# Kernel optimization log

Hardware: AMD Instinct MI355X
Metric: run time of the kernel (lower is better)

## Reference

```python
import jax, jax.numpy as jnp
import numpy as np

N = 100000   # nodes
E = 1600000  # edges (before self loops)
F = 64       # num_features
H = 64       # hidden_channels
C = 10       # num_classes
G = 128      # graphs in batch
NEG_SLOPE = 0.2


def setup_inputs() -> dict:
    key = jax.random.key(0)
    ks = jax.random.split(key, 16)
    x = jax.random.normal(ks[0], (N, F), dtype=jnp.float32)
    edge_index = jax.random.randint(ks[1], (2, E), 0, N, dtype=jnp.int64)
    batch = jnp.sort(jax.random.randint(ks[2], (N,), 0, G, dtype=jnp.int64))
    def glorot(k, shape):
        fan = shape[0] + shape[-1]
        return jax.random.uniform(k, shape, jnp.float32, -1.0, 1.0) * np.sqrt(6.0 / fan)
    return {
        "x": x, "edge_index": edge_index, "batch": batch,
        # GATConv 1 (F -> H)
        "W1": glorot(ks[3], (F, H)), "as1": glorot(ks[4], (H,)), "ad1": glorot(ks[5], (H,)), "b1": jnp.zeros((H,), jnp.float32),
        # GATConv 2 (H -> H)
        "W2": glorot(ks[6], (H, H)), "as2": glorot(ks[7], (H,)), "ad2": glorot(ks[8], (H,)), "b2": jnp.zeros((H,), jnp.float32),
        # MLP head
        "mw1": glorot(ks[9], (H, H)), "mb1": jnp.zeros((H,), jnp.float32),
        "mw2": glorot(ks[10], (H, C)), "mb2": jnp.zeros((C,), jnp.float32),
    }


def gat_conv(x, src, dst, W, a_s, a_d, b):
    # x: [N, Fin] -> h: [N, Fout]
    h = x @ W
    # per-node attention halves, gathered per edge (heads=1)
    al_s = h @ a_s   # [N]
    al_d = h @ a_d   # [N]
    e = jax.nn.leaky_relu(al_s[src] + al_d[dst], NEG_SLOPE)  # [E']
    # segment softmax over incoming edges of each destination node
    m = jax.ops.segment_max(e, dst, num_segments=N)
    ex = jnp.exp(e - m[dst])
    denom = jax.ops.segment_sum(ex, dst, num_segments=N)
    alpha = ex / denom[dst]                                   # [E']
    # weighted scatter-add of source features
    out = jax.ops.segment_sum(alpha[:, None] * h[src], dst, num_segments=N)
    return out + b


def reference(x, edge_index, batch, W1, as1, ad1, b1, W2, as2, ad2, b2, mw1, mb1, mw2, mb2):
    # add self loops (PyG GATConv default)
    loop = jnp.arange(N, dtype=edge_index.dtype)
    src = jnp.concatenate([edge_index[0], loop])
    dst = jnp.concatenate([edge_index[1], loop])

    h = gat_conv(x, src, dst, W1, as1, ad1, b1)
    h = jax.nn.elu(h)  # dropout p=0.5 is identity in eval mode
    h = gat_conv(h, src, dst, W2, as2, ad2, b2)
    h = jax.nn.elu(h)

    h = jax.nn.relu(h @ mw1 + mb1) @ mw2 + mb2   # MLP [N, C]
    return jax.ops.segment_sum(h, batch, num_segments=G)  # global_add_pool [G, C]
```

## Files before the change

### kernel.cpp

```cpp
#include <hip/hip_runtime.h>
#include <hip/hip_bf16.h>
#include <math.h>

#define SHIFT 20.0f
#define T_PER 8
#define TILE (256 * T_PER)
#define SEG_CAP 12288
#define BCAP 10240
#define LS_T 1024

typedef __bf16 bf16x8 __attribute__((ext_vector_type(8)));
typedef float  f32x4  __attribute__((ext_vector_type(4)));

__device__ __forceinline__ unsigned f2bf(float f) {
    unsigned u = __float_as_uint(f);
    return (u + 0x7fffu + ((u >> 16) & 1u)) >> 16;
}

__global__ void setup_kernel(int* __restrict__ bcur, int K2,
                             float* __restrict__ Pz, int nPz,
                             const float* __restrict__ W1,
                             const float* __restrict__ as1, const float* __restrict__ ad1,
                             const float* __restrict__ W2,
                             const float* __restrict__ as2, const float* __restrict__ ad2,
                             const float* __restrict__ mw1,
                             uint4* __restrict__ Wf1, uint4* __restrict__ Wf2,
                             uint4* __restrict__ mwf)
{
    int t = threadIdx.x;
    if (blockIdx.x == 0) {
        if (t < K2) bcur[t * 16] = t * BCAP;
        for (int i = t; i < nPz; i += 256) Pz[i] = 0.f;
        return;
    }
    __shared__ float wasad[256];
    {
        int k = t & 63;
        const float* W  = (t < 128) ? W1 : W2;
        const float* av = (t < 64) ? as1 : (t < 128) ? ad1 : (t < 192) ? as2 : ad2;
        float s = 0.f;
        for (int n = 0; n < 64; n++) s = fmaf(W[k * 64 + n], av[n], s);
        wasad[t] = s;
    }
    __syncthreads();

    for (int idx = t; idx < 1792; idx += 256) {
        const float* W; const float* wv; uint4* dst; int rem;
        if (idx < 640)       { rem = idx;        W = W1;  wv = &wasad[0];   dst = Wf1; }
        else if (idx < 1280) { rem = idx - 640;  W = W2;  wv = &wasad[128]; dst = Wf2; }
        else                 { rem = idx - 1280; W = mw1; wv = nullptr;     dst = mwf; }
        int pair = rem >> 6, l = rem & 63;
        int tt = pair >> 1, s = pair & 1;
        int kb = s * 32 + (l >> 4) * 8;
        unsigned d[4];
        if (tt < 4) {
            int n = tt * 16 + (l & 15);
            #pragma unroll
            for (int j = 0; j < 4; j++)
                d[j] = f2bf(W[(kb + 2 * j) * 64 + n]) |
                       (f2bf(W[(kb + 2 * j + 1) * 64 + n]) << 16);
        } else {
            int n0 = l & 15;
            #pragma unroll
            for (int j = 0; j < 4; j++) {
                float v0 = (n0 == 0) ? wv[kb + 2 * j]     : (n0 == 1) ? wv[64 + kb + 2 * j]     : 0.f;
                float v1 = (n0 == 0) ? wv[kb + 2 * j + 1] : (n0 == 1) ? wv[64 + kb + 2 * j + 1] : 0.f;
                d[j] = f2bf(v0) | (f2bf(v1) << 16);
            }
        }
        dst[pair * 64 + l] = make_uint4(d[0], d[1], d[2], d[3]);
    }
}

__device__ __forceinline__ void multisplit_body(
    unsigned char* lds, const int* __restrict__ esrc, const int* __restrict__ edst,
    int* __restrict__ bcur, unsigned* __restrict__ pairbuf,
    int nE, int tot, int K2, int tile)
{
    int* lhist = (int*)lds;
    int* lbase = lhist + 256;
    int t = threadIdx.x;
    int base = tile * TILE;
    if (t < K2) lhist[t] = 0;
    __syncthreads();

    unsigned pk[T_PER];
    int loc[T_PER];
    #pragma unroll
    for (int i = 0; i < T_PER; i++) {
        int e = base + t + i * 256;
        if (e < tot) {
            int s = (e < nE) ? esrc[e] : (e - nE);
            int d = (e < nE) ? edst[e] : (e - nE);
            int b = d >> 9;
            pk[i] = ((unsigned)s << 9) | (unsigned)(d & 511);
            int idx = atomicAdd(&lhist[b], 1);
            loc[i] = (b << 20) | idx;
        } else loc[i] = -1;
    }
    __syncthreads();
    if (t < K2) {
        int c = lhist[t];
        lbase[t] = (c > 0) ? atomicAdd(&bcur[t * 16], c) : 0;
    }
    __syncthreads();
    #pragma unroll
    for (int i = 0; i < T_PER; i++) {
        if (loc[i] >= 0)
            pairbuf[lbase[loc[i] >> 20] + (loc[i] & 0xFFFFF)] = pk[i];
    }
}

__device__ __forceinline__ void gemm_body(
    unsigned char* lds, const void* __restrict__ Xv, int x_is_bf16,
    const uint4* __restrict__ Wf, __hip_bfloat16* __restrict__ Hout,
    float* __restrict__ als, float* __restrict__ ald, int nN, int b0)
{
    int t = threadIdx.x, lane = t & 63, wv = t >> 6;

    uint4 wf[10];
    #pragma unroll
    for (int p = 0; p < 10; p++) wf[p] = Wf[p * 64 + lane];

    if (x_is_bf16) {
        const uint4* X4 = (const uint4*)Xv;
        int limit = nN * 8;
        #pragma unroll
        for (int k = 0; k < 8; k++) {
            int dst = t + k * 256;
            int idx = b0 * 8 + dst;
            if (idx < limit) {
                int r = dst >> 3, c = dst & 7;
                *(uint4*)(lds + r * 144 + c * 16) = X4[idx];
            }
        }
    } else {
        const float4* Xf = (const float4*)Xv;
        int limit = nN * 16;
        #pragma unroll
        for (int k = 0; k < 16; k++) {
            int dst = t + k * 256;
            int idx = b0 * 16 + dst;
            if (idx < limit) {
                float4 v = Xf[idx];
                uint2 r2;
                r2.x = f2bf(v.x) | (f2bf(v.y) << 16);
                r2.y = f2bf(v.z) | (f2bf(v.w) << 16);
                int r = dst >> 4, c = dst & 15;
                *(uint2*)(lds + r * 144 + c * 8) = r2;
            }
        }
    }
    __syncthreads();

    f32x4 acc[4][5] = {};
    int rbase = wv * 64;
    #pragma unroll
    for (int s = 0; s < 2; s++) {
        #pragma unroll
        for (int rf = 0; rf < 4; rf++) {
            const uint4 av = *(const uint4*)(lds + (rbase + rf * 16 + (lane & 15)) * 144
                                                 + s * 64 + (lane >> 4) * 16);
            bf16x8 a = __builtin_bit_cast(bf16x8, av);
            #pragma unroll
            for (int tt = 0; tt < 5; tt++) {
                bf16x8 b = __builtin_bit_cast(bf16x8, wf[tt * 2 + s]);
                acc[rf][tt] = __builtin_amdgcn_mfma_f32_16x16x32_bf16(a, b, acc[rf][tt], 0, 0, 0);
            }
        }
    }

    int q = lane >> 4, c = lane & 15;
    #pragma unroll
    for (int rf = 0; rf < 4; rf++) {
        #pragma unroll
        for (int r = 0; r < 4; r++) {
            int n = b0 + rbase + rf * 16 + q * 4 + r;
            if (n < nN) {
                #pragma unroll
                for (int tt = 0; tt < 4; tt++)
                    Hout[(size_t)n * 64 + tt * 16 + c] = __float2bfloat16(acc[rf][tt][r]);
                if (c == 0)      als[n] = acc[rf][4][r];
                else if (c == 1) ald[n] = acc[rf][4][r];
            }
        }
    }
}

__global__ __launch_bounds__(256) void ms_gemm_kernel(
    const int* __restrict__ esrc, const int* __restrict__ edst,
    int* __restrict__ bcur, unsigned* __restrict__ pairbuf,
    int nE, int nN, int K2, int nTiles,
    const void* __restrict__ Xv, const uint4* __restrict__ Wf,
    __hip_bfloat16* __restrict__ Hout,
    float* __restrict__ als, float* __restrict__ ald)
{
    __shared__ __align__(16) unsigned char lds[256 * 144];
    if (blockIdx.x < nTiles) {
        multisplit_body(lds, esrc, edst, bcur, pairbuf, nE, nE + nN, K2, blockIdx.x);
    } else {
        gemm_body(lds, Xv, 0, Wf, Hout, als, ald, nN, (blockIdx.x - nTiles) * 256);
    }
}

__global__ __launch_bounds__(256) void gemm_att_mfma(
    const void* __restrict__ Xv, int x_is_bf16,
    const uint4* __restrict__ Wf,
    __hip_bfloat16* __restrict__ Hout,
    float* __restrict__ als, float* __restrict__ ald, int nN)
{
    __shared__ __align__(16) unsigned char lds[256 * 144];
    gemm_body(lds, Xv, x_is_bf16, Wf, Hout, als, ald, nN, blockIdx.x * 256);
}

__global__ __launch_bounds__(LS_T) void local_scatter_kernel(
    const unsigned* __restrict__ pairbuf, const int* __restrict__ bcur,
    int2* __restrict__ rp2, int* __restrict__ csr_src, int nN, int K2)
{
    __shared__ unsigned seg[SEG_CAP];
    __shared__ int lh[512];
    __shared__ int cur[512];
    __shared__ int psum[512];
    int b = blockIdx.x;
    int t = threadIdx.x;
    int d0 = b * 512;
    int nd = min(512, nN - d0);
    int lo = b * BCAP;
    int hi = bcur[b * 16];
    int len = hi - lo;
    bool inLds = (len <= SEG_CAP);

    if (t < 512) lh[t] = 0;
    if (inLds)
        for (int j = t; j < len; j += LS_T) seg[j] = pairbuf[lo + j];
    __syncthreads();
    if (inLds) {
        for (int j = t; j < len; j += LS_T) atomicAdd(&lh[seg[j] & 511u], 1);
    } else {
        for (int j = lo + t; j < hi; j += LS_T)
            atomicAdd(&lh[pairbuf[j] & 511u], 1);
    }
    __syncthreads();

    int v = (t < 512) ? lh[t] : 0;
    if (t < 512) psum[t] = v;
    __syncthreads();
    for (int off = 1; off < 512; off <<= 1) {
        int u = (t < 512 && t >= off) ? psum[t - off] : 0;
        __syncthreads();
        if (t < 512) psum[t] += u;
        __syncthreads();
    }
    if (t < 512) {
        int e0 = lo + psum[t] - v;
        cur[t] = e0;
        if (t < nd) rp2[d0 + t] = make_int2(e0, v);
    }
    __syncthreads();

    if (inLds) {
        for (int j = t; j < len; j += LS_T) {
            unsigned w = seg[j];
            int pos = atomicAdd(&cur[w & 511u], 1);
            csr_src[pos] = (int)(w >> 9);
        }
    } else {
        for (int j = lo + t; j < hi; j += LS_T) {
            unsigned w = pairbuf[j];
            int pos = atomicAdd(&cur[w & 511u], 1);
            csr_src[pos] = (int)(w >> 9);
        }
    }
}

__global__ __launch_bounds__(256) void pull_kernel(
    const int* __restrict__ csr_src, const int2* __restrict__ rp2,
    const unsigned* __restrict__ Hu,
    const float* __restrict__ als, const float* __restrict__ ald,
    const float* __restrict__ bias,
    __hip_bfloat162* __restrict__ out2, int nN)
{
    int lane = threadIdx.x & 63;
    int half = lane >> 5;
    int fl = lane & 31;
    int wid  = (blockIdx.x * blockDim.x + threadIdx.x) >> 6;
    int nw   = (gridDim.x * blockDim.x) >> 6;
    float2 bl2 = ((const float2*)bias)[fl];

    for (int d = wid; d < nN; d += nw) {
        int2 rp = rp2[d];
        int s0 = rp.x, s1 = rp.x + rp.y;
        float aldd = ald[d];
        float aclo = 0.f, achi = 0.f, den = 0.f;

        for (int base = s0; base < s1; base += 64) {
            int j = base + lane;
            bool v = (j < s1);
            int sl = v ? csr_src[j] : 0;
            float ex = 0.f;
            if (v) {
                float sc = als[sl] + aldd;
                sc = (sc > 0.f) ? sc : 0.2f * sc;
                ex = __expf(sc - SHIFT);
            }
            float es = ex;
            #pragma unroll
            for (int off = 32; off > 0; off >>= 1) es += __shfl_xor(es, off);
            den += es;

            int m = min(64, s1 - base);
            int i2 = 0;
            for (; i2 + 3 < m; i2 += 4) {
                int iA = i2 + half, iB = i2 + 2 + half;
                int sA = __shfl(sl, iA), sB = __shfl(sl, iB);
                float eA = __shfl(ex, iA), eB = __shfl(ex, iB);
                unsigned dA = Hu[(size_t)sA * 32 + fl];
                unsigned dB = Hu[(size_t)sB * 32 + fl];
                aclo = fmaf(eA, __uint_as_float(dA << 16), aclo);
                achi = fmaf(eA, __uint_as_float(dA & 0xffff0000u), achi);
                aclo = fmaf(eB, __uint_as_float(dB << 16), aclo);
                achi = fmaf(eB, __uint_as_float(dB & 0xffff0000u), achi);
            }
            for (; i2 < m; i2 += 2) {
                int idx = i2 + half;
                int s = __shfl(sl, idx);
                float e = (idx < m) ? __shfl(ex, idx) : 0.f;
                unsigned dd = Hu[(size_t)s * 32 + fl];
                aclo = fmaf(e, __uint_as_float(dd << 16), aclo);
                achi = fmaf(e, __uint_as_float(dd & 0xffff0000u), achi);
            }
        }
        aclo += __shfl_xor(aclo, 32);
        achi += __shfl_xor(achi, 32);
        float v0 = aclo / den + bl2.x;
        float v1 = achi / den + bl2.y;
        v0 = (v0 > 0.f) ? v0 : expm1f(v0);
        v1 = (v1 > 0.f) ? v1 : expm1f(v1);
        if (half == 0) {
            __hip_bfloat162 pk;
            pk.x = __float2bfloat16(v0);
            pk.y = __float2bfloat16(v1);
            out2[(size_t)d * 32 + fl] = pk;
        }
    }
}

__global__ __launch_bounds__(256) void mlp_pool_mfma(
    const uint4* __restrict__ Hin,
    const uint4* __restrict__ mwf, const float* __restrict__ mb1,
    const int* __restrict__ batch,
    float* __restrict__ P, float* __restrict__ Pcnt, int nN)
{
    __shared__ __align__(16) unsigned char lds[256 * 144];
    int t = threadIdx.x, lane = t & 63, wv = t >> 6;
    int b0 = blockIdx.x * 256;

    uint4 wf[8];
    #pragma unroll
    for (int p = 0; p < 8; p++) wf[p] = mwf[p * 64 + lane];

    int limit = nN * 8;
    #pragma unroll
    for (int k = 0; k < 8; k++) {
        int dst = t + k * 256;
        int idx = b0 * 8 + dst;
        if (idx < limit) {
            int r = dst >> 3, c = dst & 7;
            *(uint4*)(lds + r * 144 + c * 16) = Hin[idx];
        }
    }
    __syncthreads();

    f32x4 acc[4][4] = {};
    int rbase = wv * 64;
    #pragma unroll
    for (int s = 0; s < 2; s++) {
        #pragma unroll
        for (int rf = 0; rf < 4; rf++) {
            const uint4 av = *(const uint4*)(lds + (rbase + rf * 16 + (lane & 15)) * 144
                                                 + s * 64 + (lane >> 4) * 16);
            bf16x8 a = __builtin_bit_cast(bf16x8, av);
            #pragma unroll
            for (int tt = 0; tt < 4; tt++) {
                bf16x8 b = __builtin_bit_cast(bf16x8, wf[tt * 2 + s]);
                acc[rf][tt] = __builtin_amdgcn_mfma_f32_16x16x32_bf16(a, b, acc[rf][tt], 0, 0, 0);
            }
        }
    }

    int q = lane >> 4, c = lane & 15;
    float bl0 = mb1[c], bl1 = mb1[16 + c], bl2 = mb1[32 + c], bl3 = mb1[48 + c];
    float r0 = 0.f, r1 = 0.f, r2 = 0.f, r3 = 0.f, ccnt = 0.f;
    int gcur = -1;
    #pragma unroll
    for (int rf = 0; rf < 4; rf++) {
        #pragma unroll
        for (int r = 0; r < 4; r++) {
            int n = b0 + rbase + rf * 16 + q * 4 + r;
            if (n < nN) {
                int g = batch[n];
                if (g != gcur) {
                    if (gcur >= 0) {
                        atomicAdd(&P[(size_t)gcur * 64 + c],      r0);
                        atomicAdd(&P[(size_t)gcur * 64 + 16 + c], r1);
                        atomicAdd(&P[(size_t)gcur * 64 + 32 + c], r2);
                        atomicAdd(&P[(size_t)gcur * 64 + 48 + c], r3);
                        if (c == 0) atomicAdd(&Pcnt[gcur], ccnt);
                    }
                    gcur = g; r0 = r1 = r2 = r3 = 0.f; ccnt = 0.f;
                }
                r0 += fmaxf(acc[rf][0][r] + bl0, 0.f);
                r1 += fmaxf(acc[rf][1][r] + bl1, 0.f);
                r2 += fmaxf(acc[rf][2][r] + bl2, 0.f);
                r3 += fmaxf(acc[rf][3][r] + bl3, 0.f);
                ccnt += 1.f;
            }
        }
    }
    if (gcur >= 0) {
        atomicAdd(&P[(size_t)gcur * 64 + c],      r0);
        atomicAdd(&P[(size_t)gcur * 64 + 16 + c], r1);
        atomicAdd(&P[(size_t)gcur * 64 + 32 + c], r2);
        atomicAdd(&P[(size_t)gcur * 64 + 48 + c], r3);
        if (c == 0) atomicAdd(&Pcnt[gcur], ccnt);
    }
}

__global__ void head_out_kernel(const float* __restrict__ P,
                                const float* __restrict__ Pcnt,
                                const float* __restrict__ mw2,
                                const float* __restrict__ mb2,
                                float* __restrict__ out, int nOut)
{
    int t = blockIdx.x * blockDim.x + threadIdx.x;
    if (t >= nOut) return;
    int g = t / 10, j = t % 10;
    float s = mb2[j] * Pcnt[g];
    const float* pr = P + (size_t)g * 64;
    #pragma unroll
    for (int k = 0; k < 64; k++) s = fmaf(pr[k], mw2[k * 10 + j], s);
    out[t] = s;
}

extern "C" void kernel_launch(void* const* d_in, const int* in_sizes, int n_in,
                              void* d_out, int out_size, void* d_ws, size_t ws_size,
                              hipStream_t stream)
{
    const float* x   = (const float*)d_in[0];
    const int*  eidx = (const int*)d_in[1];
    const int* batch = (const int*)d_in[2];
    const float* W1  = (const float*)d_in[3];
    const float* as1 = (const float*)d_in[4];
    const float* ad1 = (const float*)d_in[5];
    const float* b1  = (const float*)d_in[6];
    const float* W2  = (const float*)d_in[7];
    const float* as2 = (const float*)d_in[8];
    const float* ad2 = (const float*)d_in[9];
    const float* b2  = (const float*)d_in[10];
    const float* mw1 = (const float*)d_in[11];
    const float* mb1 = (const float*)d_in[12];
    const float* mw2 = (const float*)d_in[13];
    const float* mb2 = (const float*)d_in[14];
    float* out = (float*)d_out;

    int nN = in_sizes[0] / 64;
    int nE = in_sizes[1] / 2;
    int tot = nE + nN;
    int K2 = (nN + 511) >> 9;
    int G  = out_size / 10;
    const int* esrc = eidx;
    const int* edst = eidx + nE;

    float* ws = (float*)d_ws;
    size_t NF = (size_t)nN * 64;
    size_t capTot = (size_t)K2 * BCAP;
    float* bufA   = ws;
    float* bufB   = ws + NF;
    float* als    = ws + 2 * NF;
    float* ald    = als + nN;
    int2* rp2     = (int2*)(ald + nN);
    int* csr_src  = (int*)(rp2 + nN);
    int* bcur     = csr_src + capTot;
    float* P      = (float*)(bcur + K2 * 16 + 15);
    float* Pcnt   = P + (size_t)G * 64;
    uintptr_t wb  = ((uintptr_t)(Pcnt + G) + 255) & ~(uintptr_t)255;
    uint4* Wf1    = (uint4*)wb;
    uint4* Wf2    = Wf1 + 640;
    uint4* mwf    = Wf2 + 640;
    unsigned* pairbuf = (unsigned*)bufA;
    __hip_bfloat16* hbf = (__hip_bfloat16*)bufB;

    dim3 blk(256);
    int nTiles = (tot + TILE - 1) / TILE;
    int nT256 = (nN + 255) / 256;

    setup_kernel<<<2, blk, 0, stream>>>(bcur, K2, P, G * 64 + G,
                                        W1, as1, ad1, W2, as2, ad2, mw1,
                                        Wf1, Wf2, mwf);
    ms_gemm_kernel<<<nTiles + nT256, blk, 0, stream>>>(
        esrc, edst, bcur, pairbuf, nE, nN, K2, nTiles,
        x, Wf1, hbf, als, ald);
    local_scatter_kernel<<<K2, dim3(LS_T), 0, stream>>>(pairbuf, bcur, rp2,
                                                        csr_src, nN, K2);

    pull_kernel<<<2048, blk, 0, stream>>>(csr_src, rp2, (const unsigned*)hbf,
                                          als, ald, b1,
                                          (__hip_bfloat162*)bufA, nN);
    gemm_att_mfma<<<nT256, blk, 0, stream>>>(bufA, 1, Wf2, hbf, als, ald, nN);
    pull_kernel<<<2048, blk, 0, stream>>>(csr_src, rp2, (const unsigned*)hbf,
                                          als, ald, b2,
                                          (__hip_bfloat162*)bufA, nN);

    mlp_pool_mfma<<<nT256, blk, 0, stream>>>((const uint4*)bufA, mwf, mb1,
                                             batch, P, Pcnt, nN);
    head_out_kernel<<<(out_size + 255) / 256, blk, 0, stream>>>(P, Pcnt, mw2,
                                                                mb2, out, out_size);
}
```

Before: 302.5 us.

## Halve CSR bucket width and software-pipeline feature gathers in pull kernel

Destination buckets for the edge multisplit shrink from 512 to 256 nodes. That doubles the number of local-scatter blocks, shrinks LDS per block, and removes the global-memory overflow fallback, with lengths clamped to the bucket capacity instead. The pull kernel now prefetches the next pair of source-feature rows while accumulating the current pair, merging the tail loop into the main one. Indexing also moves from size_t to 32-bit shifts. The trade-off is that any bucket holding more than 5248 edges would spill into the next bucket and silently lose edges.

New measurement: 302.7 us. About the same (+0.0%).

```diff
diff --git a/kernel.cpp b/kernel.cpp
--- a/kernel.cpp
+++ b/kernel.cpp
@@ -5,8 +5,7 @@
 #define SHIFT 20.0f
 #define T_PER 8
 #define TILE (256 * T_PER)
-#define SEG_CAP 12288
-#define BCAP 10240
+#define BCAP 5248
 #define LS_T 1024
 
 typedef __bf16 bf16x8 __attribute__((ext_vector_type(8)));
@@ -29,7 +28,7 @@
 {
     int t = threadIdx.x;
     if (blockIdx.x == 0) {
-        if (t < K2) bcur[t * 16] = t * BCAP;
+        for (int i = t; i < K2; i += 256) bcur[i * 16] = i * BCAP;
         for (int i = t; i < nPz; i += 256) Pz[i] = 0.f;
         return;
     }
@@ -78,10 +77,10 @@
     int nE, int tot, int K2, int tile)
 {
     int* lhist = (int*)lds;
-    int* lbase = lhist + 256;
+    int* lbase = lhist + 512;
     int t = threadIdx.x;
     int base = tile * TILE;
-    if (t < K2) lhist[t] = 0;
+    for (int i = t; i < K2; i += 256) lhist[i] = 0;
     __syncthreads();
 
     unsigned pk[T_PER];
@@ -92,16 +91,16 @@
         if (e < tot) {
             int s = (e < nE) ? esrc[e] : (e - nE);
             int d = (e < nE) ? edst[e] : (e - nE);
-            int b = d >> 9;
-            pk[i] = ((unsigned)s << 9) | (unsigned)(d & 511);
+            int b = d >> 8;
+            pk[i] = ((unsigned)s << 8) | (unsigned)(d & 255);
             int idx = atomicAdd(&lhist[b], 1);
             loc[i] = (b << 20) | idx;
         } else loc[i] = -1;
     }
     __syncthreads();
-    if (t < K2) {
-        int c = lhist[t];
-        lbase[t] = (c > 0) ? atomicAdd(&bcur[t * 16], c) : 0;
+    for (int i = t; i < K2; i += 256) {
+        int c = lhist[i];
+        lbase[i] = (c > 0) ? atomicAdd(&bcur[i * 16], c) : 0;
     }
     __syncthreads();
     #pragma unroll
@@ -217,59 +216,44 @@
     const unsigned* __restrict__ pairbuf, const int* __restrict__ bcur,
     int2* __restrict__ rp2, int* __restrict__ csr_src, int nN, int K2)
 {
-    __shared__ unsigned seg[SEG_CAP];
-    __shared__ int lh[512];
-    __shared__ int cur[512];
-    __shared__ int psum[512];
+    __shared__ unsigned seg[BCAP];
+    __shared__ int lh[256];
+    __shared__ int cur[256];
+    __shared__ int psum[256];
     int b = blockIdx.x;
     int t = threadIdx.x;
-    int d0 = b * 512;
-    int nd = min(512, nN - d0);
+    int d0 = b * 256;
+    int nd = min(256, nN - d0);
     int lo = b * BCAP;
     int hi = bcur[b * 16];
-    int len = hi - lo;
-    bool inLds = (len <= SEG_CAP);
-
-    if (t < 512) lh[t] = 0;
-    if (inLds)
-        for (int j = t; j < len; j += LS_T) seg[j] = pairbuf[lo + j];
-    __syncthreads();
-    if (inLds) {
-        for (int j = t; j < len; j += LS_T) atomicAdd(&lh[seg[j] & 511u], 1);
-    } else {
-        for (int j = lo + t; j < hi; j += LS_T)
-            atomicAdd(&lh[pairbuf[j] & 511u], 1);
-    }
-    __syncthreads();
-
-    int v = (t < 512) ? lh[t] : 0;
-    if (t < 512) psum[t] = v;
-    __syncthreads();
-    for (int off = 1; off < 512; off <<= 1) {
-        int u = (t < 512 && t >= off) ? psum[t - off] : 0;
+    int len = min(hi - lo, BCAP);
+
+    if (t < 256) lh[t] = 0;
+    for (int j = t; j < len; j += LS_T) seg[j] = pairbuf[lo + j];
+    __syncthreads();
+    for (int j = t; j < len; j += LS_T) atomicAdd(&lh[seg[j] & 255u], 1);
+    __syncthreads();
+
+    int v = (t < 256) ? lh[t] : 0;
+    if (t < 256) psum[t] = v;
+    __syncthreads();
+    for (int off = 1; off < 256; off <<= 1) {
+        int u = (t < 256 && t >= off) ? psum[t - off] : 0;
         __syncthreads();
-        if (t < 512) psum[t] += u;
+        if (t < 256) psum[t] += u;
         __syncthreads();
     }
-    if (t < 512) {
+    if (t < 256) {
         int e0 = lo + psum[t] - v;
         cur[t] = e0;
         if (t < nd) rp2[d0 + t] = make_int2(e0, v);
     }
     __syncthreads();
 
-    if (inLds) {
-        for (int j = t; j < len; j += LS_T) {
-            unsigned w = seg[j];
-            int pos = atomicAdd(&cur[w & 511u], 1);
-            csr_src[pos] = (int)(w >> 9);
-        }
-    } else {
-        for (int j = lo + t; j < hi; j += LS_T) {
-            unsigned w = pairbuf[j];
-            int pos = atomicAdd(&cur[w & 511u], 1);
-            csr_src[pos] = (int)(w >> 9);
-        }
+    for (int j = t; j < len; j += LS_T) {
+        unsigned w = seg[j];
+        int pos = atomicAdd(&cur[w & 255u], 1);
+        csr_src[pos] = (int)(w >> 8);
     }
 }
 
@@ -289,14 +273,14 @@
 
     for (int d = wid; d < nN; d += nw) {
         int2 rp = rp2[d];
-        int s0 = rp.x, s1 = rp.x + rp.y;
+        int s0 = rp.x, m = rp.y;
         float aldd = ald[d];
         float aclo = 0.f, achi = 0.f, den = 0.f;
 
-        for (int base = s0; base < s1; base += 64) {
+        for (int base = 0; base < m; base += 64) {
             int j = base + lane;
-            bool v = (j < s1);
-            int sl = v ? csr_src[j] : 0;
+            bool v = (j < m);
+            int sl = v ? csr_src[s0 + j] : 0;
             float ex = 0.f;
             if (v) {
                 float sc = als[sl] + aldd;
@@ -308,26 +292,24 @@
             for (int off = 32; off > 0; off >>= 1) es += __shfl_xor(es, off);
             den += es;
 
-            int m = min(64, s1 - base);
-            int i2 = 0;
-            for (; i2 + 3 < m; i2 += 4) {
-                int iA = i2 + half, iB = i2 + 2 + half;
-                int sA = __shfl(sl, iA), sB = __shfl(sl, iB);
-                float eA = __shfl(ex, iA), eB = __shfl(ex, iB);
-                unsigned dA = Hu[(size_t)sA * 32 + fl];
-                unsigned dB = Hu[(size_t)sB * 32 + fl];
+            int mm = min(64, m - base);
+            int sA = __shfl(sl, half), sB = __shfl(sl, 2 + half);
+            float eA = __shfl(ex, half), eB = __shfl(ex, 2 + half);
+            unsigned dA = Hu[((unsigned)sA << 5) | fl];
+            unsigned dB = Hu[((unsigned)sB << 5) | fl];
+            for (int i2 = 0; i2 < mm; i2 += 4) {
+                int i4 = (i2 + 4) & 63;
+                int   sA2 = __shfl(sl, i4 + half);
+                int   sB2 = __shfl(sl, i4 + 2 + half);
+                float eA2 = __shfl(ex, i4 + half);
+                float eB2 = __shfl(ex, i4 + 2 + half);
+                unsigned dA2 = Hu[((unsigned)sA2 << 5) | fl];
+                unsigned dB2 = Hu[((unsigned)sB2 << 5) | fl];
                 aclo = fmaf(eA, __uint_as_float(dA << 16), aclo);
                 achi = fmaf(eA, __uint_as_float(dA & 0xffff0000u), achi);
                 aclo = fmaf(eB, __uint_as_float(dB << 16), aclo);
                 achi = fmaf(eB, __uint_as_float(dB & 0xffff0000u), achi);
-            }
-            for (; i2 < m; i2 += 2) {
-                int idx = i2 + half;
-                int s = __shfl(sl, idx);
-                float e = (idx < m) ? __shfl(ex, idx) : 0.f;
-                unsigned dd = Hu[(size_t)s * 32 + fl];
-                aclo = fmaf(e, __uint_as_float(dd << 16), aclo);
-                achi = fmaf(e, __uint_as_float(dd & 0xffff0000u), achi);
+                sA = sA2; sB = sB2; eA = eA2; eB = eB2; dA = dA2; dB = dB2;
             }
         }
         aclo += __shfl_xor(aclo, 32);
@@ -340,7 +322,7 @@
             __hip_bfloat162 pk;
             pk.x = __float2bfloat16(v0);
             pk.y = __float2bfloat16(v1);
-            out2[(size_t)d * 32 + fl] = pk;
+            out2[((unsigned)d << 5) | fl] = pk;
         }
     }
 }
@@ -466,7 +448,7 @@
     int nN = in_sizes[0] / 64;
     int nE = in_sizes[1] / 2;
     int tot = nE + nN;
-    int K2 = (nN + 511) >> 9;
+    int K2 = (nN + 255) >> 8;
     int G  = out_size / 10;
     const int* esrc = eidx;
     const int* edst = eidx + nE;
```
